# Kernel tuning notes

Hardware: AMD Instinct MI355X
Metric: run time of the kernel (lower is better)

The kernel has to match this reference:

```python
import jax, jax.numpy as jnp
import numpy as np

N_NODES = 50000
N_EDGES = 800000
IN_C = 116
HEADS = 4
OUT_C = 16
OUT_DIM = HEADS * OUT_C  # 64
NUM_GRAPHS = 100
NEG_SLOPE = 0.2
BN_EPS = 1e-5


def setup_inputs() -> dict:
    key = jax.random.key(0)
    ks = jax.random.split(key, 16)
    x = jax.random.normal(ks[0], (N_NODES, IN_C), dtype=jnp.float32)
    edge_index = jax.random.randint(ks[1], (2, N_EDGES), 0, N_NODES, dtype=jnp.int32)
    edge_attr = jax.random.normal(ks[2], (N_EDGES, 1), dtype=jnp.float32)
    batch = jnp.sort(jax.random.randint(ks[3], (N_NODES,), 0, NUM_GRAPHS, dtype=jnp.int32))
    s = 0.1
    return {
        "x": x, "edge_index": edge_index, "edge_attr": edge_attr, "batch": batch,
        "Wl": jax.random.normal(ks[4], (IN_C, OUT_DIM)) * s,
        "bl": jnp.zeros((OUT_DIM,), jnp.float32),
        "Wr": jax.random.normal(ks[5], (IN_C, OUT_DIM)) * s,
        "br": jnp.zeros((OUT_DIM,), jnp.float32),
        "We": jax.random.normal(ks[6], (1, OUT_DIM)) * s,
        "att": jax.random.normal(ks[7], (HEADS, OUT_C)) * s,
        "gat_bias": jnp.zeros((OUT_DIM,), jnp.float32),
        "gamma": jnp.ones((OUT_DIM,), jnp.float32),
        "beta": jnp.zeros((OUT_DIM,), jnp.float32),
        "Wres": jax.random.normal(ks[8], (IN_C, OUT_DIM)) * s,
        "bres": jnp.zeros((OUT_DIM,), jnp.float32),
        "W1": jax.random.normal(ks[9], (OUT_DIM, 64)) * s,
        "b1": jnp.zeros((64,), jnp.float32),
        "W2": jax.random.normal(ks[10], (64, 2)) * s,
        "b2": jnp.zeros((2,), jnp.float32),
    }


def _gatv2(x, edge_index, edge_attr, Wl, bl, Wr, br, We, att, gat_bias):
    N = x.shape[0]
    # linear transforms (PyG lin_l applies to source/message, lin_r to target)
    xl = (x @ Wl + bl).reshape(N, HEADS, OUT_C)
    xr = (x @ Wr + br).reshape(N, HEADS, OUT_C)
    # add self loops with fill_value=1.0 for edge_attr
    loops = jnp.arange(N, dtype=edge_index.dtype)
    src = jnp.concatenate([edge_index[0], loops])
    dst = jnp.concatenate([edge_index[1], loops])
    ea = jnp.concatenate([edge_attr, jnp.ones((N, 1), edge_attr.dtype)], axis=0)
    edge_emb = (ea @ We).reshape(-1, HEADS, OUT_C)          # [E+N, H, C]
    # GATv2 scores: att . leaky_relu(xl_j + xr_i + edge_emb)
    e = jax.nn.leaky_relu(xl[src] + xr[dst] + edge_emb, NEG_SLOPE)
    logits = jnp.einsum('ehc,hc->eh', e, att)                # [E+N, H]
    # segment softmax over incoming edges of each target node
    m = jax.ops.segment_max(logits, dst, num_segments=N)     # [N, H]
    ex = jnp.exp(logits - m[dst])
    denom = jax.ops.segment_sum(ex, dst, num_segments=N)     # [N, H]
    alpha = ex / denom[dst]
    # weighted scatter-add of source messages
    out = jax.ops.segment_sum(alpha[:, :, None] * xl[src], dst, num_segments=N)
    return out.reshape(N, OUT_DIM) + gat_bias


def reference(x, edge_index, edge_attr, batch, Wl, bl, Wr, br, We, att, gat_bias,
              gamma, beta, Wres, bres, W1, b1, W2, b2):
    h = _gatv2(x, edge_index, edge_attr, Wl, bl, Wr, br, We, att, gat_bias)
    # BatchNorm1d (training-style batch statistics over node dim)
    mu = jnp.mean(h, axis=0)
    var = jnp.var(h, axis=0)
    h = gamma * (h - mu) * jax.lax.rsqrt(var + BN_EPS) + beta
    # residual projection of original features
    h = h + (x @ Wres + bres)
    # global mean pool per graph
    sums = jax.ops.segment_sum(h, batch, num_segments=NUM_GRAPHS)
    cnts = jax.ops.segment_sum(jnp.ones((h.shape[0],), h.dtype), batch, num_segments=NUM_GRAPHS)
    pooled = sums / jnp.maximum(cnts, 1.0)[:, None]          # [G, 64]
    # 2-layer predictor with ReLU between
    z = jax.nn.relu(pooled @ W1 + b1)
    return z @ W2 + b2                                       # [G, 2]
```

## Files before the change

kernel.cpp:

```cpp
#include <hip/hip_runtime.h>
#include <hip/hip_bf16.h>

#define IN_C 116
#define HEADS 4
#define OUT_C 16
#define OUT_DIM 64
#define NEG_SLOPE 0.2f
#define BN_EPS 1e-5f
#define LIN_BM 32
#define LIN_PAD 36
#define CAP 64
#define OVF_CAP 4096
#define CYCLE 40

__global__ __launch_bounds__(256) void prep_kernel(
    const float* __restrict__ x,
    const float* __restrict__ Wl, const float* __restrict__ bl,
    const float* __restrict__ Wr, const float* __restrict__ br,
    const float* __restrict__ Wres, const float* __restrict__ bres,
    float* __restrict__ xl, float* __restrict__ xr, float* __restrict__ xres,
    const int* __restrict__ ei, const float* __restrict__ ea,
    int* __restrict__ cnt, unsigned long long* __restrict__ epack,
    int* __restrict__ ovf, int* __restrict__ ovf_cnt,
    int N, int E, int NBLIN, int FPP, int PART)
{
    __shared__ float xsT[IN_C * LIN_PAD];
    const int b = blockIdx.x;
    const int tid = threadIdx.x;

    if (b % 5 == 4) {
        const int lb = (b / CYCLE) * 8 + (b % CYCLE) / 5;
        if (lb >= NBLIN) return;
        const int bn = lb * LIN_BM;

        for (int i = tid; i < LIN_BM * IN_C; i += 256) {
            int n = i / IN_C, k = i - n * IN_C;
            int gn = bn + n;
            xsT[k * LIN_PAD + n] = (gn < N) ? x[(size_t)gn * IN_C + k] : 0.f;
        }
        __syncthreads();

        const int j = tid & 63;
        const int t = tid >> 6;
        const int nbase = 8 * t;

        float al[8] = {0,0,0,0,0,0,0,0};
        float ar[8] = {0,0,0,0,0,0,0,0};
        float as_[8] = {0,0,0,0,0,0,0,0};

        #pragma unroll 4
        for (int k = 0; k < IN_C; ++k) {
            float4 xa = *(const float4*)&xsT[k * LIN_PAD + nbase];
            float4 xb = *(const float4*)&xsT[k * LIN_PAD + nbase + 4];
            float wl  = Wl[k * OUT_DIM + j];
            float wr  = Wr[k * OUT_DIM + j];
            float wsv = Wres[k * OUT_DIM + j];
            float xv[8] = {xa.x, xa.y, xa.z, xa.w, xb.x, xb.y, xb.z, xb.w};
            #pragma unroll
            for (int u = 0; u < 8; ++u) {
                al[u]  += xv[u] * wl;
                ar[u]  += xv[u] * wr;
                as_[u] += xv[u] * wsv;
            }
        }

        float blj = bl[j], brj = br[j], bsj = bres[j];
        #pragma unroll
        for (int u = 0; u < 8; ++u) {
            int gn = bn + nbase + u;
            if (gn < N) {
                xl[(size_t)gn * OUT_DIM + j]   = al[u] + blj;
                xr[(size_t)gn * OUT_DIM + j]   = ar[u] + brj;
                xres[(size_t)gn * OUT_DIM + j] = as_[u] + bsj;
            }
        }
    } else {
        const int c = b & 7;
        const int cyc  = b / CYCLE;
        const int jcur = ((b % CYCLE) - c) >> 3;
        const int jx   = (2 * ((4 - c + 5) % 5)) % 5;
        const int q    = jcur - (jx < jcur ? 1 : 0);
        const int r    = cyc * 4 + q;

        const int lo = c * PART;
        const int hi = (lo + PART < N) ? lo + PART : N;
        const unsigned span = (unsigned)(hi - lo);

        long long e0 = (long long)r * E / FPP;
        long long e1 = (long long)(r + 1) * E / FPP;

        for (long long e = e0 + tid; e < e1; e += 256) {
            int dst = ei[E + e];
            if ((unsigned)(dst - lo) >= span) continue;
            int src = ei[e];
            float av = ea[e];
            int slot = atomicAdd(&cnt[dst], 1);
            if (slot < CAP) {
                unsigned long long v =
                    ((unsigned long long)(unsigned)__float_as_uint(av) << 32) | (unsigned)src;
                epack[(size_t)dst * CAP + slot] = v;
            } else {
                int o = atomicAdd(ovf_cnt, 1);
                if (o < OVF_CAP) {
                    ovf[3 * o] = src; ovf[3 * o + 1] = __float_as_int(av); ovf[3 * o + 2] = dst;
                }
            }
        }
    }
}

__global__ __launch_bounds__(256) void gat_gather_kernel(
    const int* __restrict__ cnt, const unsigned long long* __restrict__ epack,
    const int* __restrict__ ovf, const int* __restrict__ ovf_cnt,
    const float* __restrict__ xl, float* __restrict__ xr_hout,
    const float* __restrict__ We, const float* __restrict__ att,
    const float* __restrict__ gat_bias, int N)
{
    const int lane = threadIdx.x & 63;
    const int wv   = threadIdx.x >> 6;
    const int g    = lane >> 4;
    const int q    = lane & 15;
    const int n = blockIdx.x * 16 + wv * 4 + g;
    if (n >= N) return;

    const float4 xr4 = *(const float4*)(xr_hout + (size_t)n * OUT_DIM + 4 * q);
    const float4 We4 = *(const float4*)(We + 4 * q);
    const float4 at4 = *(const float4*)(att + 4 * q);

    int len = cnt[n];
    len = len < CAP ? len : CAP;
    const unsigned long long* ep = epack + (size_t)n * CAP;

    float den, acc0, acc1, acc2, acc3;
    {
        float4 xv = *(const float4*)(xl + (size_t)n * OUT_DIM + 4 * q);
        float s0 = xv.x + xr4.x + We4.x;
        float s1 = xv.y + xr4.y + We4.y;
        float s2 = xv.z + xr4.z + We4.z;
        float s3 = xv.w + xr4.w + We4.w;
        s0 = s0 > 0.f ? s0 : NEG_SLOPE * s0;
        s1 = s1 > 0.f ? s1 : NEG_SLOPE * s1;
        s2 = s2 > 0.f ? s2 : NEG_SLOPE * s2;
        s3 = s3 > 0.f ? s3 : NEG_SLOPE * s3;
        float pl = at4.x * s0 + at4.y * s1 + at4.z * s2 + at4.w * s3;
        pl += __shfl_xor(pl, 1);
        pl += __shfl_xor(pl, 2);
        float ex = __expf(pl);
        den = ex;
        acc0 = ex * xv.x; acc1 = ex * xv.y; acc2 = ex * xv.z; acc3 = ex * xv.w;
    }

#define EDGE_CORE(SRC, AV)                                              \
    {                                                                   \
        int src = (SRC);                                                \
        float av = (AV);                                                \
        float4 xv = *(const float4*)(xl + (size_t)src * OUT_DIM + 4*q); \
        float s0 = xv.x + xr4.x + av * We4.x;                           \
        float s1 = xv.y + xr4.y + av * We4.y;                           \
        float s2 = xv.z + xr4.z + av * We4.z;                           \
        float s3 = xv.w + xr4.w + av * We4.w;                           \
        s0 = s0 > 0.f ? s0 : NEG_SLOPE * s0;                            \
        s1 = s1 > 0.f ? s1 : NEG_SLOPE * s1;                            \
        s2 = s2 > 0.f ? s2 : NEG_SLOPE * s2;                            \
        s3 = s3 > 0.f ? s3 : NEG_SLOPE * s3;                            \
        float pl = at4.x * s0 + at4.y * s1 + at4.z * s2 + at4.w * s3;   \
        pl += __shfl_xor(pl, 1);                                        \
        pl += __shfl_xor(pl, 2);                                        \
        float ex = __expf(pl);                                          \
        den += ex;                                                      \
        acc0 += ex * xv.x;                                              \
        acc1 += ex * xv.y;                                              \
        acc2 += ex * xv.z;                                              \
        acc3 += ex * xv.w;                                              \
    }

#define EDGE_BODY(PP)                                                   \
    {                                                                   \
        unsigned long long v = __builtin_nontemporal_load(ep + (PP));   \
        EDGE_CORE((int)(unsigned)(v & 0xffffffffull),                   \
                  __uint_as_float((unsigned)(v >> 32)));                \
    }

    int p = 0;
    while (p + 8 <= len) {
        EDGE_BODY(p);     EDGE_BODY(p + 1);
        EDGE_BODY(p + 2); EDGE_BODY(p + 3);
        EDGE_BODY(p + 4); EDGE_BODY(p + 5);
        EDGE_BODY(p + 6); EDGE_BODY(p + 7);
        p += 8;
    }
    while (p + 2 <= len) { EDGE_BODY(p); EDGE_BODY(p + 1); p += 2; }
    if (p < len) EDGE_BODY(p);

    int oc = *ovf_cnt;
    if (oc > 0) {
        oc = oc < OVF_CAP ? oc : OVF_CAP;
        for (int o = 0; o < oc; ++o) {
            if (ovf[3 * o + 2] == n)
                EDGE_CORE(ovf[3 * o], __int_as_float(ovf[3 * o + 1]));
        }
    }
#undef EDGE_BODY
#undef EDGE_CORE

    const float4 bias4 = *(const float4*)(gat_bias + 4 * q);
    float inv = 1.0f / den;
    float4 o;
    o.x = acc0 * inv + bias4.x;
    o.y = acc1 * inv + bias4.y;
    o.z = acc2 * inv + bias4.z;
    o.w = acc3 * inv + bias4.w;
    *(float4*)(xr_hout + (size_t)n * OUT_DIM + 4 * q) = o;
}

__global__ __launch_bounds__(256) void stats_kernel(
    const float* __restrict__ h, float* __restrict__ chansum,
    float* __restrict__ chansumsq, int N)
{
    const int j = threadIdx.x & 63;
    const int t = threadIdx.x >> 6;
    float s = 0.f, ss = 0.f;
    for (int n = blockIdx.x * 4 + t; n < N; n += gridDim.x * 4) {
        float v = h[(size_t)n * OUT_DIM + j];
        s += v; ss += v * v;
    }
    __shared__ float ls[4][64], lss[4][64];
    ls[t][j] = s; lss[t][j] = ss;
    __syncthreads();
    if (t == 0) {
        atomicAdd(&chansum[j],   ls[0][j] + ls[1][j] + ls[2][j] + ls[3][j]);
        atomicAdd(&chansumsq[j], lss[0][j] + lss[1][j] + lss[2][j] + lss[3][j]);
    }
}

__global__ __launch_bounds__(256) void bn_res_pool_kernel(
    const float* __restrict__ hraw, const float* __restrict__ xres,
    const float* __restrict__ chansum, const float* __restrict__ chansumsq,
    const float* __restrict__ gamma, const float* __restrict__ beta,
    const int* __restrict__ batch,
    float* __restrict__ pooled, float* __restrict__ cnt, int N)
{
    const int j = threadIdx.x & 63;
    const int t = threadIdx.x >> 6;
    const int base = blockIdx.x * 256;
    const float invN = 1.0f / (float)N;
    const float mj = chansum[j] * invN;
    const float var = chansumsq[j] * invN - mj * mj;
    const float rj = rsqrtf(var + BN_EPS);
    const float gj = gamma[j], bj = beta[j];

    float sum = 0.f, c = 0.f;
    int gcur = -1;
    for (int i = t; i < 256; i += 4) {
        int n = base + i;
        if (n >= N) break;
        int g = batch[n];
        if (g != gcur) {
            if (gcur >= 0) {
                atomicAdd(&pooled[gcur * OUT_DIM + j], sum);
                if (j == 0) atomicAdd(&cnt[gcur], c);
            }
            sum = 0.f; c = 0.f; gcur = g;
        }
        float v = gj * (hraw[(size_t)n * OUT_DIM + j] - mj) * rj + bj
                + xres[(size_t)n * OUT_DIM + j];
        sum += v; c += 1.f;
    }
    if (gcur >= 0) {
        atomicAdd(&pooled[gcur * OUT_DIM + j], sum);
        if (j == 0) atomicAdd(&cnt[gcur], c);
    }
}

__global__ __launch_bounds__(64) void mlp_kernel(
    const float* __restrict__ pooled, const float* __restrict__ cnt,
    const float* __restrict__ W1, const float* __restrict__ b1,
    const float* __restrict__ W2, const float* __restrict__ b2,
    float* __restrict__ out, int G)
{
    int g = blockIdx.x, j = threadIdx.x;
    __shared__ float ps[64];
    float c = cnt[g];
    c = c > 1.0f ? c : 1.0f;
    ps[j] = pooled[g * OUT_DIM + j] / c;
    __syncthreads();
    float z = b1[j];
    for (int k = 0; k < 64; ++k) z += ps[k] * W1[k * 64 + j];
    z = z > 0.f ? z : 0.f;
    float o0 = z * W2[j * 2 + 0];
    float o1 = z * W2[j * 2 + 1];
    #pragma unroll
    for (int off = 32; off > 0; off >>= 1) {
        o0 += __shfl_down(o0, off);
        o1 += __shfl_down(o1, off);
    }
    if (j == 0) {
        out[g * 2 + 0] = o0 + b2[0];
        out[g * 2 + 1] = o1 + b2[1];
    }
}

extern "C" void kernel_launch(void* const* d_in, const int* in_sizes, int n_in,
                              void* d_out, int out_size, void* d_ws, size_t ws_size,
                              hipStream_t stream) {
    const float* x        = (const float*)d_in[0];
    const int*   ei       = (const int*)d_in[1];
    const float* ea       = (const float*)d_in[2];
    const int*   batch    = (const int*)d_in[3];
    const float* Wl       = (const float*)d_in[4];
    const float* bl       = (const float*)d_in[5];
    const float* Wr       = (const float*)d_in[6];
    const float* br       = (const float*)d_in[7];
    const float* We       = (const float*)d_in[8];
    const float* att      = (const float*)d_in[9];
    const float* gat_bias = (const float*)d_in[10];
    const float* gamma    = (const float*)d_in[11];
    const float* beta     = (const float*)d_in[12];
    const float* Wres     = (const float*)d_in[13];
    const float* bres     = (const float*)d_in[14];
    const float* W1       = (const float*)d_in[15];
    const float* b1       = (const float*)d_in[16];
    const float* W2       = (const float*)d_in[17];
    const float* b2       = (const float*)d_in[18];
    float* out = (float*)d_out;

    const int N = in_sizes[0] / IN_C;
    const int E = in_sizes[1] / 2;
    const int G = out_size / 2;

    float* ws = (float*)d_ws;
    float* xl      = ws;
    float* xr      = xl + (size_t)N * OUT_DIM;
    float* xres    = xr + (size_t)N * OUT_DIM;
    unsigned long long* epack =
        (unsigned long long*)(xres + (size_t)N * OUT_DIM);
    int*   cnt     = (int*)(epack + (size_t)N * CAP);
    int*   ovf_cnt = cnt + N;
    float* chansum   = (float*)(ovf_cnt + 1);
    float* chansumsq = chansum + 64;
    float* pooled    = chansumsq + 64;
    float* cntg      = pooled + (size_t)G * OUT_DIM;
    int*   ovf       = (int*)(cntg + G);

    size_t zero_bytes = (size_t)((char*)(cntg + G) - (char*)cnt);
    hipMemsetAsync(cnt, 0, zero_bytes, stream);

    const int NBLIN = (N + LIN_BM - 1) / LIN_BM;
    const int CYC   = (NBLIN + 7) / 8;
    const int T     = CYC * CYCLE;
    const int FPP   = CYC * 4;
    const int PART  = (N + 7) / 8;

    prep_kernel<<<T, 256, 0, stream>>>(
        x, Wl, bl, Wr, br, Wres, bres, xl, xr, xres,
        ei, ea, cnt, epack, ovf, ovf_cnt, N, E, NBLIN, FPP, PART);

    gat_gather_kernel<<<(N + 15) / 16, 256, 0, stream>>>(
        cnt, epack, ovf, ovf_cnt, xl, xr, We, att, gat_bias, N);

    stats_kernel<<<256, 256, 0, stream>>>(xr, chansum, chansumsq, N);

    bn_res_pool_kernel<<<(N + 255) / 256, 256, 0, stream>>>(
        xr, xres, chansum, chansumsq, gamma, beta, batch, pooled, cntg, N);

    mlp_kernel<<<G, 64, 0, stream>>>(pooled, cntg, W1, b1, W2, b2, out, G);
}
```

Before: 271.0 us.

## Fuse BN stats into gather, shrink edge CAP, repartition fill into quarters

Result: slower. 324.7 us (+19.8%).

```diff
diff --git a/kernel.cpp b/kernel.cpp
--- a/kernel.cpp
+++ b/kernel.cpp
@@ -9,7 +9,7 @@
 #define BN_EPS 1e-5f
 #define LIN_BM 32
 #define LIN_PAD 36
-#define CAP 64
+#define CAP 32
 #define OVF_CAP 4096
 #define CYCLE 40
 
@@ -27,9 +27,10 @@
     __shared__ float xsT[IN_C * LIN_PAD];
     const int b = blockIdx.x;
     const int tid = threadIdx.x;
-
-    if (b % 5 == 4) {
-        const int lb = (b / CYCLE) * 8 + (b % CYCLE) / 5;
+    const int m = b % CYCLE;
+
+    if (m % 5 == 4) {
+        const int lb = (b / CYCLE) * 8 + m / 5;
         if (lb >= NBLIN) return;
         const int bn = lb * LIN_BM;
 
@@ -75,12 +76,12 @@
             }
         }
     } else {
-        const int c = b & 7;
-        const int cyc  = b / CYCLE;
-        const int jcur = ((b % CYCLE) - c) >> 3;
-        const int jx   = (2 * ((4 - c + 5) % 5)) % 5;
-        const int q    = jcur - (jx < jcur ? 1 : 0);
-        const int r    = cyc * 4 + q;
+        const int c = b & 3;
+        const int cyc = b / CYCLE;
+        const int k   = m >> 2;
+        const int k0  = (c + 1) % 5;
+        const int q   = k - (k > k0 ? 1 : 0) - (k > k0 + 5 ? 1 : 0);
+        const int r   = cyc * 8 + q;
 
         const int lo = c * PART;
         const int hi = (lo + PART < N) ? lo + PART : N;
@@ -89,23 +90,41 @@
         long long e0 = (long long)r * E / FPP;
         long long e1 = (long long)(r + 1) * E / FPP;
 
-        for (long long e = e0 + tid; e < e1; e += 256) {
-            int dst = ei[E + e];
-            if ((unsigned)(dst - lo) >= span) continue;
-            int src = ei[e];
-            float av = ea[e];
-            int slot = atomicAdd(&cnt[dst], 1);
-            if (slot < CAP) {
-                unsigned long long v =
-                    ((unsigned long long)(unsigned)__float_as_uint(av) << 32) | (unsigned)src;
-                epack[(size_t)dst * CAP + slot] = v;
-            } else {
-                int o = atomicAdd(ovf_cnt, 1);
-                if (o < OVF_CAP) {
-                    ovf[3 * o] = src; ovf[3 * o + 1] = __float_as_int(av); ovf[3 * o + 2] = dst;
-                }
-            }
-        }
+#define FILL_ONE(EE, DST)                                                     \
+        if ((unsigned)((DST) - lo) < span) {                                  \
+            int src = ei[EE];                                                 \
+            float av = ea[EE];                                                \
+            int slot = atomicAdd(&cnt[DST], 1);                               \
+            if (slot < CAP) {                                                 \
+                unsigned long long v =                                        \
+                    ((unsigned long long)(unsigned)__float_as_uint(av) << 32) \
+                    | (unsigned)src;                                          \
+                epack[(size_t)(DST) * CAP + slot] = v;                        \
+            } else {                                                          \
+                int o = atomicAdd(ovf_cnt, 1);                                \
+                if (o < OVF_CAP) {                                            \
+                    ovf[3 * o] = src; ovf[3 * o + 1] = __float_as_int(av);    \
+                    ovf[3 * o + 2] = (DST);                                   \
+                }                                                             \
+            }                                                                 \
+        }
+
+        long long e = e0 + tid;
+        for (; e + 768 < e1; e += 1024) {
+            int d0 = ei[E + e];
+            int d1 = ei[E + e + 256];
+            int d2 = ei[E + e + 512];
+            int d3 = ei[E + e + 768];
+            FILL_ONE(e,       d0);
+            FILL_ONE(e + 256, d1);
+            FILL_ONE(e + 512, d2);
+            FILL_ONE(e + 768, d3);
+        }
+        for (; e < e1; e += 256) {
+            int d = ei[E + e];
+            FILL_ONE(e, d);
+        }
+#undef FILL_ONE
     }
 }
 
@@ -114,122 +133,131 @@
     const int* __restrict__ ovf, const int* __restrict__ ovf_cnt,
     const float* __restrict__ xl, float* __restrict__ xr_hout,
     const float* __restrict__ We, const float* __restrict__ att,
-    const float* __restrict__ gat_bias, int N)
+    const float* __restrict__ gat_bias,
+    float* __restrict__ chansum, float* __restrict__ chansumsq, int N)
 {
     const int lane = threadIdx.x & 63;
     const int wv   = threadIdx.x >> 6;
     const int g    = lane >> 4;
     const int q    = lane & 15;
     const int n = blockIdx.x * 16 + wv * 4 + g;
-    if (n >= N) return;
-
-    const float4 xr4 = *(const float4*)(xr_hout + (size_t)n * OUT_DIM + 4 * q);
-    const float4 We4 = *(const float4*)(We + 4 * q);
-    const float4 at4 = *(const float4*)(att + 4 * q);
-
-    int len = cnt[n];
-    len = len < CAP ? len : CAP;
-    const unsigned long long* ep = epack + (size_t)n * CAP;
-
-    float den, acc0, acc1, acc2, acc3;
-    {
-        float4 xv = *(const float4*)(xl + (size_t)n * OUT_DIM + 4 * q);
-        float s0 = xv.x + xr4.x + We4.x;
-        float s1 = xv.y + xr4.y + We4.y;
-        float s2 = xv.z + xr4.z + We4.z;
-        float s3 = xv.w + xr4.w + We4.w;
-        s0 = s0 > 0.f ? s0 : NEG_SLOPE * s0;
-        s1 = s1 > 0.f ? s1 : NEG_SLOPE * s1;
-        s2 = s2 > 0.f ? s2 : NEG_SLOPE * s2;
-        s3 = s3 > 0.f ? s3 : NEG_SLOPE * s3;
-        float pl = at4.x * s0 + at4.y * s1 + at4.z * s2 + at4.w * s3;
-        pl += __shfl_xor(pl, 1);
-        pl += __shfl_xor(pl, 2);
-        float ex = __expf(pl);
-        den = ex;
-        acc0 = ex * xv.x; acc1 = ex * xv.y; acc2 = ex * xv.z; acc3 = ex * xv.w;
-    }
+    const bool valid = (n < N);
+
+    float4 o = make_float4(0.f, 0.f, 0.f, 0.f);
+
+    if (valid) {
+        const float4 xr4 = *(const float4*)(xr_hout + (size_t)n * OUT_DIM + 4 * q);
+        const float4 We4 = *(const float4*)(We + 4 * q);
+        const float4 at4 = *(const float4*)(att + 4 * q);
+
+        int len = cnt[n];
+        len = len < CAP ? len : CAP;
+        const unsigned long long* ep = epack + (size_t)n * CAP;
+
+        float den, acc0, acc1, acc2, acc3;
+        {
+            float4 xv = *(const float4*)(xl + (size_t)n * OUT_DIM + 4 * q);
+            float s0 = xv.x + xr4.x + We4.x;
+            float s1 = xv.y + xr4.y + We4.y;
+            float s2 = xv.z + xr4.z + We4.z;
+            float s3 = xv.w + xr4.w + We4.w;
+            s0 = s0 > 0.f ? s0 : NEG_SLOPE * s0;
+            s1 = s1 > 0.f ? s1 : NEG_SLOPE * s1;
+            s2 = s2 > 0.f ? s2 : NEG_SLOPE * s2;
+            s3 = s3 > 0.f ? s3 : NEG_SLOPE * s3;
+            float pl = at4.x * s0 + at4.y * s1 + at4.z * s2 + at4.w * s3;
+            pl += __shfl_xor(pl, 1);
+            pl += __shfl_xor(pl, 2);
+            float ex = __expf(pl);
+            den = ex;
+            acc0 = ex * xv.x; acc1 = ex * xv.y; acc2 = ex * xv.z; acc3 = ex * xv.w;
+        }
 
 #define EDGE_CORE(SRC, AV)                                              \
-    {                                                                   \
-        int src = (SRC);                                                \
-        float av = (AV);                                                \
-        float4 xv = *(const float4*)(xl + (size_t)src * OUT_DIM + 4*q); \
-        float s0 = xv.x + xr4.x + av * We4.x;                           \
-        float s1 = xv.y + xr4.y + av * We4.y;                           \
-        float s2 = xv.z + xr4.z + av * We4.z;                           \
-        float s3 = xv.w + xr4.w + av * We4.w;                           \
-        s0 = s0 > 0.f ? s0 : NEG_SLOPE * s0;                            \
-        s1 = s1 > 0.f ? s1 : NEG_SLOPE * s1;                            \
-        s2 = s2 > 0.f ? s2 : NEG_SLOPE * s2;                            \
-        s3 = s3 > 0.f ? s3 : NEG_SLOPE * s3;                            \
-        float pl = at4.x * s0 + at4.y * s1 + at4.z * s2 + at4.w * s3;   \
-        pl += __shfl_xor(pl, 1);                                        \
-        pl += __shfl_xor(pl, 2);                                        \
-        float ex = __expf(pl);                                          \
-        den += ex;                                                      \
-        acc0 += ex * xv.x;                                              \
-        acc1 += ex * xv.y;                                              \
-        acc2 += ex * xv.z;                                              \
-        acc3 += ex * xv.w;                                              \
-    }
+        {                                                               \
+            int src = (SRC);                                            \
+            float av = (AV);                                            \
+            float4 xv = *(const float4*)(xl + (size_t)src * OUT_DIM + 4*q); \
+            float s0 = xv.x + xr4.x + av * We4.x;                       \
+            float s1 = xv.y + xr4.y + av * We4.y;                       \
+            float s2 = xv.z + xr4.z + av * We4.z;                       \
+            float s3 = xv.w + xr4.w + av * We4.w;                       \
+            s0 = s0 > 0.f ? s0 : NEG_SLOPE * s0;                        \
+            s1 = s1 > 0.f ? s1 : NEG_SLOPE * s1;                        \
+            s2 = s2 > 0.f ? s2 : NEG_SLOPE * s2;                        \
+            s3 = s3 > 0.f ? s3 : NEG_SLOPE * s3;                        \
+            float pl = at4.x * s0 + at4.y * s1 + at4.z * s2 + at4.w * s3; \
+            pl += __shfl_xor(pl, 1);                                    \
+            pl += __shfl_xor(pl, 2);                                    \
+            float ex = __expf(pl);                                      \
+            den += ex;                                                  \
+            acc0 += ex * xv.x;                                          \
+            acc1 += ex * xv.y;                                          \
+            acc2 += ex * xv.z;                                          \
+            acc3 += ex * xv.w;                                          \
+        }
 
 #define EDGE_BODY(PP)                                                   \
-    {                                                                   \
-        unsigned long long v = __builtin_nontemporal_load(ep + (PP));   \
-        EDGE_CORE((int)(unsigned)(v & 0xffffffffull),                   \
-                  __uint_as_float((unsigned)(v >> 32)));                \
-    }
-
-    int p = 0;
-    while (p + 8 <= len) {
-        EDGE_BODY(p);     EDGE_BODY(p + 1);
-        EDGE_BODY(p + 2); EDGE_BODY(p + 3);
-        EDGE_BODY(p + 4); EDGE_BODY(p + 5);
-        EDGE_BODY(p + 6); EDGE_BODY(p + 7);
-        p += 8;
-    }
-    while (p + 2 <= len) { EDGE_BODY(p); EDGE_BODY(p + 1); p += 2; }
-    if (p < len) EDGE_BODY(p);
-
-    int oc = *ovf_cnt;
-    if (oc > 0) {
-        oc = oc < OVF_CAP ? oc : OVF_CAP;
-        for (int o = 0; o < oc; ++o) {
-            if (ovf[3 * o + 2] == n)
-                EDGE_CORE(ovf[3 * o], __int_as_float(ovf[3 * o + 1]));
-        }
-    }
+        {                                                               \
+            unsigned long long v = ep[PP];                              \
+            EDGE_CORE((int)(unsigned)(v & 0xffffffffull),               \
+                      __uint_as_float((unsigned)(v >> 32)));            \
+        }
+
+        int p = 0;
+        while (p + 8 <= len) {
+            EDGE_BODY(p);     EDGE_BODY(p + 1);
+            EDGE_BODY(p + 2); EDGE_BODY(p + 3);
+            EDGE_BODY(p + 4); EDGE_BODY(p + 5);
+            EDGE_BODY(p + 6); EDGE_BODY(p + 7);
+            p += 8;
+        }
+        while (p + 2 <= len) { EDGE_BODY(p); EDGE_BODY(p + 1); p += 2; }
+        if (p < len) EDGE_BODY(p);
+
+        int oc = *ovf_cnt;
+        if (oc > 0) {
+            oc = oc < OVF_CAP ? oc : OVF_CAP;
+            for (int ov = 0; ov < oc; ++ov) {
+                if (ovf[3 * ov + 2] == n)
+                    EDGE_CORE(ovf[3 * ov], __int_as_float(ovf[3 * ov + 1]));
+            }
+        }
 #undef EDGE_BODY
 #undef EDGE_CORE
 
-    const float4 bias4 = *(const float4*)(gat_bias + 4 * q);
-    float inv = 1.0f / den;
-    float4 o;
-    o.x = acc0 * inv + bias4.x;
-    o.y = acc1 * inv + bias4.y;
-    o.z = acc2 * inv + bias4.z;
-    o.w = acc3 * inv + bias4.w;
-    *(float4*)(xr_hout + (size_t)n * OUT_DIM + 4 * q) = o;
-}
-
-__global__ __launch_bounds__(256) void stats_kernel(
-    const float* __restrict__ h, float* __restrict__ chansum,
-    float* __restrict__ chansumsq, int N)
-{
-    const int j = threadIdx.x & 63;
-    const int t = threadIdx.x >> 6;
-    float s = 0.f, ss = 0.f;
-    for (int n = blockIdx.x * 4 + t; n < N; n += gridDim.x * 4) {
-        float v = h[(size_t)n * OUT_DIM + j];
-        s += v; ss += v * v;
-    }
-    __shared__ float ls[4][64], lss[4][64];
-    ls[t][j] = s; lss[t][j] = ss;
+        const float4 bias4 = *(const float4*)(gat_bias + 4 * q);
+        float inv = 1.0f / den;
+        o.x = acc0 * inv + bias4.x;
+        o.y = acc1 * inv + bias4.y;
+        o.z = acc2 * inv + bias4.z;
+        o.w = acc3 * inv + bias4.w;
+        *(float4*)(xr_hout + (size_t)n * OUT_DIM + 4 * q) = o;
+    }
+
+    float s0 = o.x, s1 = o.y, s2 = o.z, s3 = o.w;
+    float t0 = o.x*o.x, t1 = o.y*o.y, t2 = o.z*o.z, t3 = o.w*o.w;
+    #pragma unroll
+    for (int mask = 16; mask <= 32; mask <<= 1) {
+        s0 += __shfl_xor(s0, mask); s1 += __shfl_xor(s1, mask);
+        s2 += __shfl_xor(s2, mask); s3 += __shfl_xor(s3, mask);
+        t0 += __shfl_xor(t0, mask); t1 += __shfl_xor(t1, mask);
+        t2 += __shfl_xor(t2, mask); t3 += __shfl_xor(t3, mask);
+    }
+    __shared__ float sm_s[4][16][4], sm_t[4][16][4];
+    if (lane < 16) {
+        sm_s[wv][q][0] = s0; sm_s[wv][q][1] = s1;
+        sm_s[wv][q][2] = s2; sm_s[wv][q][3] = s3;
+        sm_t[wv][q][0] = t0; sm_t[wv][q][1] = t1;
+        sm_t[wv][q][2] = t2; sm_t[wv][q][3] = t3;
+    }
     __syncthreads();
-    if (t == 0) {
-        atomicAdd(&chansum[j],   ls[0][j] + ls[1][j] + ls[2][j] + ls[3][j]);
-        atomicAdd(&chansumsq[j], lss[0][j] + lss[1][j] + lss[2][j] + lss[3][j]);
+    if (threadIdx.x < 64) {
+        int qq = threadIdx.x >> 2, ii = threadIdx.x & 3;
+        float S = sm_s[0][qq][ii] + sm_s[1][qq][ii] + sm_s[2][qq][ii] + sm_s[3][qq][ii];
+        float T = sm_t[0][qq][ii] + sm_t[1][qq][ii] + sm_t[2][qq][ii] + sm_t[3][qq][ii];
+        atomicAdd(&chansum[threadIdx.x], S);
+        atomicAdd(&chansumsq[threadIdx.x], T);
     }
 }
 
@@ -348,17 +376,16 @@
     const int NBLIN = (N + LIN_BM - 1) / LIN_BM;
     const int CYC   = (NBLIN + 7) / 8;
     const int T     = CYC * CYCLE;
-    const int FPP   = CYC * 4;
-    const int PART  = (N + 7) / 8;
+    const int FPP   = CYC * 8;
+    const int PART  = (N + 3) / 4;
 
     prep_kernel<<<T, 256, 0, stream>>>(
         x, Wl, bl, Wr, br, Wres, bres, xl, xr, xres,
         ei, ea, cnt, epack, ovf, ovf_cnt, N, E, NBLIN, FPP, PART);
 
     gat_gather_kernel<<<(N + 15) / 16, 256, 0, stream>>>(
-        cnt, epack, ovf, ovf_cnt, xl, xr, We, att, gat_bias, N);
-
-    stats_kernel<<<256, 256, 0, stream>>>(xr, chansum, chansumsq, N);
+        cnt, epack, ovf, ovf_cnt, xl, xr, We, att, gat_bias,
+        chansum, chansumsq, N);
 
     bn_res_pool_kernel<<<(N + 255) / 256, 256, 0, stream>>>(
         xr, xres, chansum, chansumsq, gamma, beta, batch, pooled, cntg, N);
```

## Halve edge bucket capacity, repartition fill into 4 node ranges, batch dst loads

Applied to the files above, without the earlier changes.

New measurement: 272.8 us. No clear change (+0.7%).

```diff
diff --git a/kernel.cpp b/kernel.cpp
--- a/kernel.cpp
+++ b/kernel.cpp
@@ -9,7 +9,7 @@
 #define BN_EPS 1e-5f
 #define LIN_BM 32
 #define LIN_PAD 36
-#define CAP 64
+#define CAP 32
 #define OVF_CAP 4096
 #define CYCLE 40
 
@@ -27,9 +27,10 @@
     __shared__ float xsT[IN_C * LIN_PAD];
     const int b = blockIdx.x;
     const int tid = threadIdx.x;
-
-    if (b % 5 == 4) {
-        const int lb = (b / CYCLE) * 8 + (b % CYCLE) / 5;
+    const int m = b % CYCLE;
+
+    if (m % 5 == 4) {
+        const int lb = (b / CYCLE) * 8 + m / 5;
         if (lb >= NBLIN) return;
         const int bn = lb * LIN_BM;
 
@@ -75,12 +76,12 @@
             }
         }
     } else {
-        const int c = b & 7;
-        const int cyc  = b / CYCLE;
-        const int jcur = ((b % CYCLE) - c) >> 3;
-        const int jx   = (2 * ((4 - c + 5) % 5)) % 5;
-        const int q    = jcur - (jx < jcur ? 1 : 0);
-        const int r    = cyc * 4 + q;
+        const int c = b & 3;
+        const int cyc = b / CYCLE;
+        const int k   = m >> 2;
+        const int k0  = (c + 1) % 5;
+        const int q   = k - (k > k0 ? 1 : 0) - (k > k0 + 5 ? 1 : 0);
+        const int r   = cyc * 8 + q;
 
         const int lo = c * PART;
         const int hi = (lo + PART < N) ? lo + PART : N;
@@ -89,23 +90,41 @@
         long long e0 = (long long)r * E / FPP;
         long long e1 = (long long)(r + 1) * E / FPP;
 
-        for (long long e = e0 + tid; e < e1; e += 256) {
-            int dst = ei[E + e];
-            if ((unsigned)(dst - lo) >= span) continue;
-            int src = ei[e];
-            float av = ea[e];
-            int slot = atomicAdd(&cnt[dst], 1);
-            if (slot < CAP) {
-                unsigned long long v =
-                    ((unsigned long long)(unsigned)__float_as_uint(av) << 32) | (unsigned)src;
-                epack[(size_t)dst * CAP + slot] = v;
-            } else {
-                int o = atomicAdd(ovf_cnt, 1);
-                if (o < OVF_CAP) {
-                    ovf[3 * o] = src; ovf[3 * o + 1] = __float_as_int(av); ovf[3 * o + 2] = dst;
-                }
-            }
-        }
+#define FILL_ONE(EE, DST)                                                     \
+        if ((unsigned)((DST) - lo) < span) {                                  \
+            int src = ei[EE];                                                 \
+            float av = ea[EE];                                                \
+            int slot = atomicAdd(&cnt[DST], 1);                               \
+            if (slot < CAP) {                                                 \
+                unsigned long long v =                                        \
+                    ((unsigned long long)(unsigned)__float_as_uint(av) << 32) \
+                    | (unsigned)src;                                          \
+                epack[(size_t)(DST) * CAP + slot] = v;                        \
+            } else {                                                          \
+                int o = atomicAdd(ovf_cnt, 1);                                \
+                if (o < OVF_CAP) {                                            \
+                    ovf[3 * o] = src; ovf[3 * o + 1] = __float_as_int(av);    \
+                    ovf[3 * o + 2] = (DST);                                   \
+                }                                                             \
+            }                                                                 \
+        }
+
+        long long e = e0 + tid;
+        for (; e + 768 < e1; e += 1024) {
+            int d0 = ei[E + e];
+            int d1 = ei[E + e + 256];
+            int d2 = ei[E + e + 512];
+            int d3 = ei[E + e + 768];
+            FILL_ONE(e,       d0);
+            FILL_ONE(e + 256, d1);
+            FILL_ONE(e + 512, d2);
+            FILL_ONE(e + 768, d3);
+        }
+        for (; e < e1; e += 256) {
+            int d = ei[E + e];
+            FILL_ONE(e, d);
+        }
+#undef FILL_ONE
     }
 }
 
@@ -176,7 +195,7 @@
 
 #define EDGE_BODY(PP)                                                   \
     {                                                                   \
-        unsigned long long v = __builtin_nontemporal_load(ep + (PP));   \
+        unsigned long long v = ep[PP];                                  \
         EDGE_CORE((int)(unsigned)(v & 0xffffffffull),                   \
                   __uint_as_float((unsigned)(v >> 32)));                \
     }
@@ -348,8 +367,8 @@
     const int NBLIN = (N + LIN_BM - 1) / LIN_BM;
     const int CYC   = (NBLIN + 7) / 8;
     const int T     = CYC * CYCLE;
-    const int FPP   = CYC * 4;
-    const int PART  = (N + 7) / 8;
+    const int FPP   = CYC * 8;
+    const int PART  = (N + 3) / 4;
 
     prep_kernel<<<T, 256, 0, stream>>>(
         x, Wl, bl, Wr, br, Wres, bres, xl, xr, xres,
```
